# Kernel tuning notes

Hardware: AMD Instinct MI355X
Metric: run time of the kernel (lower is better)

Reference implementation:

```python
import jax, jax.numpy as jnp
import numpy as np

DIM = 1024
NQ = 16
NKV = 4
HD = DIM // NQ  # 64
HID = 2048
E = 8
B, S = 1, 1024
EPS = 1e-6


def rmsnorm(x, w):
    ms = jnp.mean(x * x, axis=-1, keepdims=True)
    return w * (x * jax.lax.rsqrt(ms + EPS))


def rope_tables(seq_len, head_dim):
    inv_freq = 1.0 / (10000.0 ** (jnp.arange(0, head_dim, 2, dtype=jnp.float32) / head_dim))
    t = jnp.arange(seq_len, dtype=jnp.float32)
    freqs = jnp.einsum('i,j->ij', t, inv_freq)  # [S, HD/2]
    return jnp.cos(freqs), jnp.sin(freqs)


def apply_rope(x, cos, sin):
    # x: [B, S, H, HD]; cos/sin: [S, HD/2]
    c = cos[None, :, None, :]
    s = sin[None, :, None, :]
    half = x.shape[-1] // 2
    x1, x2 = x[..., :half], x[..., half:]
    return jnp.concatenate([x1 * c - x2 * s, x1 * s + x2 * c], axis=-1)


def setup_inputs() -> dict:
    key = jax.random.key(0)
    ks = jax.random.split(key, 20)
    sc = lambda fan_in: 1.0 / np.sqrt(fan_in)
    d = {}
    d['x'] = jax.random.normal(ks[0], (B, S, DIM), dtype=jnp.float32)
    d['ln1_w'] = jnp.ones((DIM,), jnp.float32)
    d['ln2_w'] = jnp.ones((DIM,), jnp.float32)
    d['Wq'] = jax.random.normal(ks[1], (DIM, DIM), jnp.float32) * sc(DIM)
    d['bq'] = jnp.zeros((DIM,), jnp.float32)
    d['Wk'] = jax.random.normal(ks[2], (DIM, HD * NKV), jnp.float32) * sc(DIM)
    d['bk'] = jnp.zeros((HD * NKV,), jnp.float32)
    d['Wv'] = jax.random.normal(ks[3], (DIM, HD * NKV), jnp.float32) * sc(DIM)
    d['bv'] = jnp.zeros((HD * NKV,), jnp.float32)
    d['qn_w'] = jnp.ones((HD,), jnp.float32)
    d['kn_w'] = jnp.ones((HD,), jnp.float32)
    d['Wg'] = jax.random.normal(ks[4], (HD, HD), jnp.float32) * sc(HD)
    d['bg'] = jnp.zeros((HD,), jnp.float32)
    d['Wo'] = jax.random.normal(ks[5], (DIM, DIM), jnp.float32) * sc(DIM)
    d['bo'] = jnp.zeros((DIM,), jnp.float32)
    d['Wr'] = jax.random.normal(ks[6], (DIM, E), jnp.float32) * sc(DIM)
    d['br'] = jnp.zeros((E,), jnp.float32)
    d['W1'] = jax.random.normal(ks[7], (E, DIM, 2 * HID), jnp.float32) * sc(DIM)
    d['b1'] = jnp.zeros((E, 2 * HID), jnp.float32)
    d['W2'] = jax.random.normal(ks[8], (E, HID, DIM), jnp.float32) * sc(HID)
    d['b2'] = jnp.zeros((E, DIM), jnp.float32)
    return d


def _forward(x, ln1_w, ln2_w, Wq, bq, Wk, bk, Wv, bv, qn_w, kn_w, Wg, bg, Wo, bo,
             Wr, br, W1, b1, W2, b2):
    batch, seq, _ = x.shape
    cos, sin = rope_tables(seq, HD)

    # --- attention ---
    h = rmsnorm(x, ln1_w)
    q = (h @ Wq + bq).reshape(batch, seq, NQ, HD)
    k = (h @ Wk + bk).reshape(batch, seq, NKV, HD)
    v = (h @ Wv + bv).reshape(batch, seq, NKV, HD)
    q = rmsnorm(apply_rope(q, cos, sin), qn_w)
    k = rmsnorm(apply_rope(k, cos, sin), kn_w)
    rep = NQ // NKV
    k = jnp.repeat(k, rep, axis=2)  # [B,S,NQ,HD]
    v = jnp.repeat(v, rep, axis=2)
    scores = jnp.einsum('bthd,bshd->bhts', q, k) / np.sqrt(HD)
    causal = jnp.tril(jnp.ones((seq, seq), dtype=bool))
    scores = jnp.where(causal[None, None], scores, -jnp.inf)
    attn = jax.nn.softmax(scores, axis=-1)
    out = jnp.einsum('bhts,bshd->bthd', attn, v)
    gate = jax.nn.sigmoid(out @ Wg + bg)
    out = (out * gate).reshape(batch, seq, DIM)
    x = x + out @ Wo + bo

    # --- top-1 MoE (note: output is NOT scaled by router probs) ---
    h2 = rmsnorm(x, ln2_w)
    logits = h2 @ Wr + br  # [B,S,E]
    top1 = jnp.argmax(logits, axis=-1).reshape(-1)  # [T]
    xt = h2.reshape(-1, DIM)  # [T,DIM]
    # dense dispatch: run all experts, gather the chosen one
    u = jnp.einsum('td,edf->tef', xt, W1) + b1  # [T,E,2H]
    u1, u2 = u[..., :HID], u[..., HID:]
    act = u1 * jax.nn.sigmoid(u2)  # SwiGLU
    y_all = jnp.einsum('teh,ehd->ted', act, W2) + b2  # [T,E,DIM]
    y = jnp.take_along_axis(y_all, top1[:, None, None], axis=1)[:, 0, :]
    return x + y.reshape(batch, seq, DIM)


def reference(x, ln1_w, ln2_w, Wq, bq, Wk, bk, Wv, bv, qn_w, kn_w, Wg, bg, Wo, bo,
              Wr, br, W1, b1, W2, b2):
    return _forward(x, ln1_w, ln2_w, Wq, bq, Wk, bk, Wv, bv, qn_w, kn_w,
                    Wg, bg, Wo, bo, Wr, br, W1, b1, W2, b2)
```

## Files before the change

kernel.cpp:

```cpp
#include <hip/hip_runtime.h>
#include <hip/hip_bf16.h>
#include <cstddef>

#define DIM 1024
#define NQ 16
#define NKV 4
#define HD 64
#define HID 2048
#define NE 8
#define SEQ 1024
#define EPSF 1e-6f
#define MAX_TILES 24
#define GST 72

typedef __hip_bfloat16 bf16;
typedef __attribute__((ext_vector_type(8))) short short8;
typedef __attribute__((ext_vector_type(4))) float floatx4;

typedef union { short8 s; unsigned int u[4]; } s8u;

__device__ __forceinline__ unsigned int f2b(float f) {
    union { bf16 b; unsigned short s; } u;
    u.b = __float2bfloat16(f);
    return (unsigned int)u.s;
}
__device__ __forceinline__ unsigned int pk2(float a, float b) {
    return f2b(a) | (f2b(b) << 16);
}

__device__ __forceinline__ void touch_f32(const float* __restrict__ p,
                                          size_t nlines, size_t gid, size_t step)
{
    float acc = 0.f;
    for (size_t i = gid; i < nlines; i += step)
        acc += p[i << 5];
    asm volatile("" :: "v"(acc));
}

__global__ __launch_bounds__(256) void rmsnorm_kernel(const float* __restrict__ src,
                                                      const float* __restrict__ w,
                                                      float* __restrict__ dst)
{
    int row = blockIdx.x, tid = threadIdx.x;
    __shared__ float red[256];
    float vals[4];
    float sq = 0.f;
    size_t base = (size_t)row * DIM;
    #pragma unroll
    for (int i = 0; i < 4; i++) {
        int idx = tid + i * 256;
        float v = src[base + idx];
        vals[i] = v; sq += v * v;
    }
    red[tid] = sq; __syncthreads();
    for (int s = 128; s > 0; s >>= 1) {
        if (tid < s) red[tid] += red[tid + s];
        __syncthreads();
    }
    float rs = 1.0f / sqrtf(red[0] * (1.0f / DIM) + EPSF);
    #pragma unroll
    for (int i = 0; i < 4; i++) {
        int idx = tid + i * 256;
        dst[base + idx] = w[idx] * vals[i] * rs;
    }
}

template<int NB>
__global__ __launch_bounds__(256) void gemm_t(
    const float* __restrict__ A, const float* __restrict__ B, const float* __restrict__ bias,
    float* __restrict__ C, const float* __restrict__ resf,
    const int* __restrict__ perm, const int* __restrict__ tile_expert,
    int N, int K, int mode)
{
    constexpr int KR = NB / 4;
    constexpr int NT = NB / 16;
    __shared__ short As[64 * GST];
    __shared__ short Bs[NB * GST];
    int tid = threadIdx.x;
    int mbase = blockIdx.y * 64, nbase = blockIdx.x * NB;

    size_t Beoff = 0, biasoff = 0;
    if (tile_expert) {
        int e = tile_expert[blockIdx.y];
        if (e < 0) return;
        Beoff = (size_t)e * K * N;
        biasoff = (size_t)e * N;
    }

    int ar = tid >> 4, ak = (tid & 15) << 2;
    int bn = tid & (NB - 1), bkk = (tid / NB) * KR;
    const float* BpBase = B + Beoff + (size_t)bkk * N + nbase + bn;

    int wv = tid >> 6, ln = tid & 63;
    int fm = (wv << 4) + (ln & 15);
    int fn = ln & 15;
    int fk = (ln >> 4) << 3;

    floatx4 acc[NT];
    #pragma unroll
    for (int nt = 0; nt < NT; nt++)
        #pragma unroll
        for (int r = 0; r < 4; r++) acc[nt][r] = 0.f;

    float4 apre[4];
    float bpre[KR];
    #pragma unroll
    for (int p = 0; p < 4; p++)
        apre[p] = *(const float4*)(A + (size_t)(mbase + (p << 4) + ar) * K + ak);
    #pragma unroll
    for (int i = 0; i < KR; i++)
        bpre[i] = BpBase[(size_t)i * N];

    for (int kt = 0; kt < K; kt += 64) {
        #pragma unroll
        for (int p = 0; p < 4; p++) {
            int m = (p << 4) + ar;
            uint2 wpk; wpk.x = pk2(apre[p].x, apre[p].y); wpk.y = pk2(apre[p].z, apre[p].w);
            *(uint2*)&As[m * GST + ak] = wpk;
        }
        #pragma unroll
        for (int i2 = 0; i2 < KR; i2 += 8) {
            unsigned int u[4];
            #pragma unroll
            for (int i = 0; i < 4; i++)
                u[i] = pk2(bpre[i2 + 2 * i], bpre[i2 + 2 * i + 1]);
            *(uint4*)&Bs[bn * GST + bkk + i2] = make_uint4(u[0], u[1], u[2], u[3]);
        }
        __syncthreads();

        int kn = kt + 64;
        if (kn < K) {
            #pragma unroll
            for (int p = 0; p < 4; p++)
                apre[p] = *(const float4*)(A + (size_t)(mbase + (p << 4) + ar) * K + kn + ak);
            const float* bp = BpBase + (size_t)kn * N;
            #pragma unroll
            for (int i = 0; i < KR; i++) bpre[i] = bp[(size_t)i * N];
        }

        #pragma unroll
        for (int ks = 0; ks < 2; ks++) {
            short8 af = *(const short8*)&As[fm * GST + (ks << 5) + fk];
            #pragma unroll
            for (int nt = 0; nt < NT; nt++) {
                short8 bf = *(const short8*)&Bs[((nt << 4) + fn) * GST + (ks << 5) + fk];
                acc[nt] = __builtin_amdgcn_mfma_f32_16x16x32_bf16(af, bf, acc[nt], 0, 0, 0);
            }
        }
        __syncthreads();
    }

    int rowb = mbase + (wv << 4) + ((ln >> 4) << 2);
    if (mode == 2) {
        int tk[4];
        #pragma unroll
        for (int r = 0; r < 4; r++) tk[r] = perm[rowb + r];
        #pragma unroll
        for (int nt = 0; nt < NT; nt++) {
            int col = nbase + (nt << 4) + fn;
            float bsv = bias[biasoff + col];
            #pragma unroll
            for (int r = 0; r < 4; r++)
                if (tk[r] >= 0)
                    C[(size_t)tk[r] * N + col] = resf[(size_t)tk[r] * N + col] + acc[nt][r] + bsv;
        }
    } else {
        #pragma unroll
        for (int nt = 0; nt < NT; nt++) {
            int col = nbase + (nt << 4) + fn;
            float bsv = bias[col];
            #pragma unroll
            for (int r = 0; r < 4; r++) {
                float vv = acc[nt][r] + bsv;
                if (mode == 1) vv += resf[(size_t)(rowb + r) * N + col];
                C[(size_t)(rowb + r) * N + col] = vv;
            }
        }
    }
}

__global__ __launch_bounds__(256) void qkv_kernel(
    const float* __restrict__ A,
    const float* __restrict__ Wq, const float* __restrict__ bq,
    const float* __restrict__ Wk, const float* __restrict__ bk,
    const float* __restrict__ Wv, const float* __restrict__ bv,
    const float* __restrict__ Wwarm,
    float* __restrict__ qo, float* __restrict__ ko, float* __restrict__ vo)
{
    constexpr int NB = 32, KR = 8, NT = 2;
    int tid = threadIdx.x;
    int bx = blockIdx.x;

    if (bx >= 48) {
        size_t gid  = ((size_t)(bx - 48) * gridDim.y + blockIdx.y) * 256 + tid;
        size_t step = (size_t)64 * gridDim.y * 256;
        touch_f32(Wwarm, (size_t)NE * DIM * (2 * HID) / 32, gid, step);
        return;
    }

    __shared__ short As[64 * GST];
    __shared__ short Bs[NB * GST];
    int mbase = blockIdx.y * 64;

    const float* B; const float* bias; float* C; int N, nbase;
    if (bx < 32)      { B = Wq; bias = bq; C = qo; N = DIM;      nbase = bx * 32; }
    else if (bx < 40) { B = Wk; bias = bk; C = ko; N = NKV * HD; nbase = (bx - 32) * 32; }
    else              { B = Wv; bias = bv; C = vo; N = NKV * HD; nbase = (bx - 40) * 32; }

    int ar = tid >> 4, ak = (tid & 15) << 2;
    int bn = tid & (NB - 1), bkk = (tid / NB) * KR;
    const float* BpBase = B + (size_t)bkk * N + nbase + bn;

    int wv = tid >> 6, ln = tid & 63;
    int fm = (wv << 4) + (ln & 15);
    int fn = ln & 15;
    int fk = (ln >> 4) << 3;

    floatx4 acc[NT];
    #pragma unroll
    for (int nt = 0; nt < NT; nt++)
        #pragma unroll
        for (int r = 0; r < 4; r++) acc[nt][r] = 0.f;

    float4 apre[4];
    float bpre[KR];
    #pragma unroll
    for (int p = 0; p < 4; p++)
        apre[p] = *(const float4*)(A + (size_t)(mbase + (p << 4) + ar) * DIM + ak);
    #pragma unroll
    for (int i = 0; i < KR; i++)
        bpre[i] = BpBase[(size_t)i * N];

    for (int kt = 0; kt < DIM; kt += 64) {
        #pragma unroll
        for (int p = 0; p < 4; p++) {
            int m = (p << 4) + ar;
            uint2 wpk; wpk.x = pk2(apre[p].x, apre[p].y); wpk.y = pk2(apre[p].z, apre[p].w);
            *(uint2*)&As[m * GST + ak] = wpk;
        }
        {
            unsigned int u[4];
            #pragma unroll
            for (int i = 0; i < 4; i++)
                u[i] = pk2(bpre[2 * i], bpre[2 * i + 1]);
            *(uint4*)&Bs[bn * GST + bkk] = make_uint4(u[0], u[1], u[2], u[3]);
        }
        __syncthreads();

        int kn = kt + 64;
        if (kn < DIM) {
            #pragma unroll
            for (int p = 0; p < 4; p++)
                apre[p] = *(const float4*)(A + (size_t)(mbase + (p << 4) + ar) * DIM + kn + ak);
            const float* bp = BpBase + (size_t)kn * N;
            #pragma unroll
            for (int i = 0; i < KR; i++) bpre[i] = bp[(size_t)i * N];
        }

        #pragma unroll
        for (int ks = 0; ks < 2; ks++) {
            short8 af = *(const short8*)&As[fm * GST + (ks << 5) + fk];
            #pragma unroll
            for (int nt = 0; nt < NT; nt++) {
                short8 bf = *(const short8*)&Bs[((nt << 4) + fn) * GST + (ks << 5) + fk];
                acc[nt] = __builtin_amdgcn_mfma_f32_16x16x32_bf16(af, bf, acc[nt], 0, 0, 0);
            }
        }
        __syncthreads();
    }

    int rowb = mbase + (wv << 4) + ((ln >> 4) << 2);
    #pragma unroll
    for (int nt = 0; nt < NT; nt++) {
        int col = nbase + (nt << 4) + fn;
        float bsv = bias[col];
        #pragma unroll
        for (int r = 0; r < 4; r++)
            C[(size_t)(rowb + r) * N + col] = acc[nt][r] + bsv;
    }
}

__global__ __launch_bounds__(256) void moe1_kernel(
    const float* __restrict__ A,
    const float* __restrict__ W1,
    const float* __restrict__ b1,
    float* __restrict__ act,
    const int* __restrict__ perm,
    const int* __restrict__ tile_expert)
{
    constexpr int NB = 32, KR = 8, NT = 2;
    __shared__ short As[64 * GST];
    __shared__ short B1s[NB * GST];
    __shared__ short B2s[NB * GST];
    int tid = threadIdx.x;
    int mbase = blockIdx.y * 64, nbase = blockIdx.x * NB;
    int e = tile_expert[blockIdx.y];
    if (e < 0) return;
    const float* Wp = W1 + (size_t)e * DIM * (2 * HID);
    const float* bp1 = b1 + (size_t)e * (2 * HID);

    int ar = tid >> 4, ak = (tid & 15) << 2;
    int tok[4];
    #pragma unroll
    for (int p = 0; p < 4; p++) tok[p] = perm[mbase + (p << 4) + ar];

    int bn = tid & (NB - 1), bkk = (tid / NB) * KR;
    const float* BpBase = Wp + (size_t)bkk * (2 * HID) + nbase + bn;

    int wv = tid >> 6, ln = tid & 63;
    int fm = (wv << 4) + (ln & 15);
    int fn = ln & 15;
    int fk = (ln >> 4) << 3;

    floatx4 acc1[NT], acc2[NT];
    #pragma unroll
    for (int nt = 0; nt < NT; nt++)
        #pragma unroll
        for (int r = 0; r < 4; r++) { acc1[nt][r] = 0.f; acc2[nt][r] = 0.f; }

    float4 apre[4];
    float b1pre[KR], b2pre[KR];
    #pragma unroll
    for (int p = 0; p < 4; p++)
        apre[p] = (tok[p] >= 0)
            ? *(const float4*)(A + (size_t)tok[p] * DIM + ak)
            : make_float4(0.f, 0.f, 0.f, 0.f);
    #pragma unroll
    for (int i = 0; i < KR; i++) {
        b1pre[i] = BpBase[(size_t)i * (2 * HID)];
        b2pre[i] = BpBase[(size_t)i * (2 * HID) + HID];
    }

    for (int kt = 0; kt < DIM; kt += 64) {
        #pragma unroll
        for (int p = 0; p < 4; p++) {
            int m = (p << 4) + ar;
            uint2 wpk; wpk.x = pk2(apre[p].x, apre[p].y); wpk.y = pk2(apre[p].z, apre[p].w);
            *(uint2*)&As[m * GST + ak] = wpk;
        }
        {
            unsigned int u1[4], u2[4];
            #pragma unroll
            for (int i = 0; i < 4; i++) {
                u1[i] = pk2(b1pre[2 * i], b1pre[2 * i + 1]);
                u2[i] = pk2(b2pre[2 * i], b2pre[2 * i + 1]);
            }
            *(uint4*)&B1s[bn * GST + bkk] = make_uint4(u1[0], u1[1], u1[2], u1[3]);
            *(uint4*)&B2s[bn * GST + bkk] = make_uint4(u2[0], u2[1], u2[2], u2[3]);
        }
        __syncthreads();

        int kn = kt + 64;
        if (kn < DIM) {
            #pragma unroll
            for (int p = 0; p < 4; p++)
                apre[p] = (tok[p] >= 0)
                    ? *(const float4*)(A + (size_t)tok[p] * DIM + kn + ak)
                    : make_float4(0.f, 0.f, 0.f, 0.f);
            const float* bp = BpBase + (size_t)kn * (2 * HID);
            #pragma unroll
            for (int i = 0; i < KR; i++) {
                b1pre[i] = bp[(size_t)i * (2 * HID)];
                b2pre[i] = bp[(size_t)i * (2 * HID) + HID];
            }
        }

        #pragma unroll
        for (int ks = 0; ks < 2; ks++) {
            short8 af = *(const short8*)&As[fm * GST + (ks << 5) + fk];
            #pragma unroll
            for (int nt = 0; nt < NT; nt++) {
                int bo = ((nt << 4) + fn) * GST + (ks << 5) + fk;
                short8 bf1 = *(const short8*)&B1s[bo];
                short8 bf2 = *(const short8*)&B2s[bo];
                acc1[nt] = __builtin_amdgcn_mfma_f32_16x16x32_bf16(af, bf1, acc1[nt], 0, 0, 0);
                acc2[nt] = __builtin_amdgcn_mfma_f32_16x16x32_bf16(af, bf2, acc2[nt], 0, 0, 0);
            }
        }
        __syncthreads();
    }

    int rowb = mbase + (wv << 4) + ((ln >> 4) << 2);
    #pragma unroll
    for (int nt = 0; nt < NT; nt++) {
        int col = nbase + (nt << 4) + fn;
        float bs1 = bp1[col];
        float bs2 = bp1[HID + col];
        #pragma unroll
        for (int r = 0; r < 4; r++) {
            float u1 = acc1[nt][r] + bs1;
            float u2 = acc2[nt][r] + bs2;
            act[(size_t)(rowb + r) * HID + col] = u1 * (1.0f / (1.0f + expf(-u2)));
        }
    }
}

__global__ __launch_bounds__(64) void rope_rms_kernel(float* __restrict__ qb,
                                                      float* __restrict__ kb,
                                                      const float* __restrict__ qnw,
                                                      const float* __restrict__ knw)
{
    int t = blockIdx.x, hy = blockIdx.y, d = threadIdx.x;
    float* x; const float* w; int nh, h;
    if (hy < NQ) { x = qb; w = qnw; nh = NQ;  h = hy; }
    else         { x = kb; w = knw; nh = NKV; h = hy - NQ; }
    int base = (t * nh + h) * HD;
    int i = d & 31;
    float x1 = x[base + i];
    float x2 = x[base + 32 + i];
    float inv = 1.0f / powf(10000.0f, (float)(2 * i) * (1.0f / HD));
    float fr = (float)t * inv;
    float c = cosf(fr), s = sinf(fr);
    float r = (d < 32) ? (x1 * c - x2 * s) : (x1 * s + x2 * c);
    float sq = r * r;
    #pragma unroll
    for (int m = 32; m >= 1; m >>= 1) sq += __shfl_xor(sq, m);
    float rs = 1.0f / sqrtf(sq * (1.0f / HD) + EPSF);
    __syncthreads();
    x[base + d] = r * rs * w[d];
}

__global__ __launch_bounds__(256) void fattn_kernel(const float* __restrict__ q,
                                                    const float* __restrict__ k,
                                                    const float* __restrict__ v,
                                                    const float* __restrict__ Wg,
                                                    const float* __restrict__ bg,
                                                    const float* __restrict__ W2warm,
                                                    float* __restrict__ o)
{
    int h = blockIdx.x;
    int tid = threadIdx.x;

    if (h >= NQ) {
        size_t gid  = ((size_t)(h - NQ) * gridDim.y + blockIdx.y) * 256 + tid;
        size_t step = (size_t)32 * gridDim.y * 256;
        touch_f32(W2warm, (size_t)NE * HID * DIM / 32, gid, step);
        return;
    }

    __shared__ short lds[2][2][64 * GST];

    int qt = blockIdx.y;
    int kvh = h >> 2;
    int w = tid >> 6, ln = tid & 63;
    int c = ln & 15, g = ln >> 4;
    int qbase = qt * 64;
    const size_t krow = (size_t)NKV * HD;

    short8 qf[2];
    {
        const float* qp = q + ((size_t)(qbase + 16 * w + c) * NQ + h) * HD + 8 * g;
        #pragma unroll
        for (int ks = 0; ks < 2; ks++) {
            float4 a = *(const float4*)(qp + 32 * ks);
            float4 b = *(const float4*)(qp + 32 * ks + 4);
            s8u t;
            t.u[0] = pk2(a.x * 0.125f, a.y * 0.125f);
            t.u[1] = pk2(a.z * 0.125f, a.w * 0.125f);
            t.u[2] = pk2(b.x * 0.125f, b.y * 0.125f);
            t.u[3] = pk2(b.z * 0.125f, b.w * 0.125f);
            qf[ks] = t.s;
        }
    }

    int kr[4], kd4[4];
    #pragma unroll
    for (int i = 0; i < 4; i++) { int f4 = tid + 256 * i; kr[i] = f4 >> 4; kd4[i] = f4 & 15; }
    int vd = tid & 63, vrb = (tid >> 6) << 4;

    float4 kreg[4];
    float vreg[16];
    {
        const float* kb = k + (size_t)kvh * HD;
        #pragma unroll
        for (int i = 0; i < 4; i++)
            kreg[i] = *(const float4*)(kb + (size_t)kr[i] * krow + kd4[i] * 4);
        const float* vb = v + (size_t)kvh * HD + vd;
        #pragma unroll
        for (int i = 0; i < 16; i++)
            vreg[i] = vb[(size_t)(vrb + i) * krow];
    }

    float m_i = -INFINITY, l_i = 0.f;
    floatx4 ot[4];
    #pragma unroll
    for (int mt = 0; mt < 4; mt++)
        #pragma unroll
        for (int r = 0; r < 4; r++) ot[mt][r] = 0.f;

    for (int kt = 0; kt <= qt; kt++) {
        short* KB = lds[kt & 1][0];
        short* VT = lds[kt & 1][1];

        #pragma unroll
        for (int i = 0; i < 4; i++) {
            uint2 wp; wp.x = pk2(kreg[i].x, kreg[i].y); wp.y = pk2(kreg[i].z, kreg[i].w);
            *(uint2*)&KB[kr[i] * GST + kd4[i] * 4] = wp;
        }
        {
            unsigned int u[8];
            #pragma unroll
            for (int i = 0; i < 8; i++) u[i] = pk2(vreg[2 * i], vreg[2 * i + 1]);
            *(uint4*)&VT[vd * GST + vrb]     = make_uint4(u[0], u[1], u[2], u[3]);
            *(uint4*)&VT[vd * GST + vrb + 8] = make_uint4(u[4], u[5], u[6], u[7]);
        }
        __syncthreads();

        if (kt < qt) {
            int kb2 = (kt + 1) * 64;
            const float* kb = k + ((size_t)kb2 * NKV + kvh) * HD;
            #pragma unroll
            for (int i = 0; i < 4; i++)
                kreg[i] = *(const float4*)(kb + (size_t)kr[i] * krow + kd4[i] * 4);
            const float* vp = v + ((size_t)kb2 * NKV + kvh) * HD + vd;
            #pragma unroll
            for (int i = 0; i < 16; i++)
                vreg[i] = vp[(size_t)(vrb + i) * krow];
        }

        float p[4][4];
        #pragma unroll
        for (int mt = 0; mt < 4; mt++) {
            floatx4 s = {0.f, 0.f, 0.f, 0.f};
            #pragma unroll
            for (int ks = 0; ks < 2; ks++) {
                short8 kf = *(const short8*)&KB[(16 * mt + c) * GST + 32 * ks + 8 * g];
                s = __builtin_amdgcn_mfma_f32_16x16x32_bf16(kf, qf[ks], s, 0, 0, 0);
            }
            #pragma unroll
            for (int r = 0; r < 4; r++) p[mt][r] = s[r];
        }

        if (kt == qt) {
            #pragma unroll
            for (int mt = 0; mt < 4; mt++)
                #pragma unroll
                for (int r = 0; r < 4; r++)
                    if (16 * mt + 4 * g + r > 16 * w + c) p[mt][r] = -1e30f;
        }

        float tm = p[0][0];
        #pragma unroll
        for (int mt = 0; mt < 4; mt++)
            #pragma unroll
            for (int r = 0; r < 4; r++) tm = fmaxf(tm, p[mt][r]);
        tm = fmaxf(tm, __shfl_xor(tm, 16));
        tm = fmaxf(tm, __shfl_xor(tm, 32));
        float mn = fmaxf(m_i, tm);
        float alpha = __expf(m_i - mn);
        float ts = 0.f;
        #pragma unroll
        for (int mt = 0; mt < 4; mt++)
            #pragma unroll
            for (int r = 0; r < 4; r++) {
                float e = __expf(p[mt][r] - mn);
                p[mt][r] = e; ts += e;
            }
        ts += __shfl_xor(ts, 16);
        ts += __shfl_xor(ts, 32);
        l_i = alpha * l_i + ts;
        m_i = mn;
        #pragma unroll
        for (int mt = 0; mt < 4; mt++)
            #pragma unroll
            for (int r = 0; r < 4; r++) ot[mt][r] *= alpha;

        unsigned int pd[4][2];
        #pragma unroll
        for (int mt = 0; mt < 4; mt++) {
            pd[mt][0] = pk2(p[mt][0], p[mt][1]);
            pd[mt][1] = pk2(p[mt][2], p[mt][3]);
        }

        int srcA = c + ((ln & 16) << 1);
        int srcB = srcA + 16;
        int gh = g >> 1;
        short8 pf[2];
        #pragma unroll
        for (int ks = 0; ks < 2; ks++) {
            s8u t;
            unsigned int a0 = (unsigned)__shfl((int)pd[2 * ks][0],     srcA);
            unsigned int a1 = (unsigned)__shfl((int)pd[2 * ks + 1][0], srcA);
            t.u[0] = gh ? a1 : a0;
            unsigned int b0 = (unsigned)__shfl((int)pd[2 * ks][1],     srcA);
            unsigned int b1 = (unsigned)__shfl((int)pd[2 * ks + 1][1], srcA);
            t.u[1] = gh ? b1 : b0;
            unsigned int c0 = (unsigned)__shfl((int)pd[2 * ks][0],     srcB);
            unsigned int c1 = (unsigned)__shfl((int)pd[2 * ks + 1][0], srcB);
            t.u[2] = gh ? c1 : c0;
            unsigned int d0 = (unsigned)__shfl((int)pd[2 * ks][1],     srcB);
            unsigned int d1 = (unsigned)__shfl((int)pd[2 * ks + 1][1], srcB);
            t.u[3] = gh ? d1 : d0;
            pf[ks] = t.s;
        }

        #pragma unroll
        for (int mt = 0; mt < 4; mt++) {
            #pragma unroll
            for (int ks = 0; ks < 2; ks++) {
                short8 vf = *(const short8*)&VT[(16 * mt + c) * GST + 32 * ks + 8 * g];
                ot[mt] = __builtin_amdgcn_mfma_f32_16x16x32_bf16(vf, pf[ks], ot[mt], 0, 0, 0);
            }
        }
    }

    __syncthreads();
    float* L   = (float*)lds;
    float* WgS = L + 64 * 68;

    int we = tid >> 2, wd = (tid & 3) << 4;
    float4 wg4[4];
    #pragma unroll
    for (int i = 0; i < 4; i++)
        wg4[i] = *(const float4*)(Wg + (size_t)we * HD + wd + 4 * i);

    float rl = 1.0f / l_i;
    #pragma unroll
    for (int mt = 0; mt < 4; mt++)
        #pragma unroll
        for (int r = 0; r < 4; r++)
            L[(16 * w + c) * 68 + 16 * mt + 4 * g + r] = ot[mt][r] * rl;
    #pragma unroll
    for (int i = 0; i < 4; i++)
        *(float4*)&WgS[we * 68 + wd + 4 * i] = wg4[i];
    __syncthreads();

    int r = tid >> 2, d0 = (tid & 3) << 4;
    float4 a0 = *(const float4*)(bg + d0);
    float4 a1 = *(const float4*)(bg + d0 + 4);
    float4 a2 = *(const float4*)(bg + d0 + 8);
    float4 a3 = *(const float4*)(bg + d0 + 12);
    for (int e = 0; e < HD; e++) {
        float ov = L[r * 68 + e];
        float4 w0 = *(const float4*)&WgS[e * 68 + d0];
        float4 w1 = *(const float4*)&WgS[e * 68 + d0 + 4];
        float4 w2 = *(const float4*)&WgS[e * 68 + d0 + 8];
        float4 w3 = *(const float4*)&WgS[e * 68 + d0 + 12];
        a0.x += ov * w0.x; a0.y += ov * w0.y; a0.z += ov * w0.z; a0.w += ov * w0.w;
        a1.x += ov * w1.x; a1.y += ov * w1.y; a1.z += ov * w1.z; a1.w += ov * w1.w;
        a2.x += ov * w2.x; a2.y += ov * w2.y; a2.z += ov * w2.z; a2.w += ov * w2.w;
        a3.x += ov * w3.x; a3.y += ov * w3.y; a3.z += ov * w3.z; a3.w += ov * w3.w;
    }
    float* op = o + ((size_t)(qbase + r) * NQ + h) * HD + d0;
    float4 av[4] = {a0, a1, a2, a3};
    #pragma unroll
    for (int i = 0; i < 4; i++) {
        float4 ov4 = *(const float4*)&L[r * 68 + d0 + 4 * i];
        float4 res;
        res.x = ov4.x / (1.0f + expf(-av[i].x));
        res.y = ov4.y / (1.0f + expf(-av[i].y));
        res.z = ov4.z / (1.0f + expf(-av[i].z));
        res.w = ov4.w / (1.0f + expf(-av[i].w));
        *(float4*)(op + 4 * i) = res;
    }
}

__global__ __launch_bounds__(64) void router_kernel(const float* __restrict__ h2,
                                                    const float* __restrict__ Wr,
                                                    const float* __restrict__ br,
                                                    int* __restrict__ top1)
{
    int t = blockIdx.x, lane = threadIdx.x;
    float acc[NE] = {0.f, 0.f, 0.f, 0.f, 0.f, 0.f, 0.f, 0.f};
    for (int d = lane; d < DIM; d += 64) {
        float hv = h2[(size_t)t * DIM + d];
        float4 w0 = *(const float4*)(Wr + (size_t)d * NE);
        float4 w1 = *(const float4*)(Wr + (size_t)d * NE + 4);
        acc[0] += hv * w0.x; acc[1] += hv * w0.y;
        acc[2] += hv * w0.z; acc[3] += hv * w0.w;
        acc[4] += hv * w1.x; acc[5] += hv * w1.y;
        acc[6] += hv * w1.z; acc[7] += hv * w1.w;
    }
    #pragma unroll
    for (int e = 0; e < NE; e++)
        for (int off = 32; off >= 1; off >>= 1) acc[e] += __shfl_down(acc[e], off);
    if (lane == 0) {
        float best = acc[0] + br[0]; int be = 0;
        #pragma unroll
        for (int e = 1; e < NE; e++) {
            float l = acc[e] + br[e];
            if (l > best) { best = l; be = e; }
        }
        top1[t] = be;
    }
}

__global__ __launch_bounds__(64) void bucket_kernel(const int* __restrict__ top1,
                                                    int* __restrict__ perm,
                                                    int* __restrict__ tile_expert)
{
    int lane = threadIdx.x;

    int e_of[16];
    {
        const int4* tp = (const int4*)(top1 + lane * 16);
        #pragma unroll
        for (int c = 0; c < 4; c++) {
            int4 v = tp[c];
            e_of[c * 4 + 0] = v.x & 7;
            e_of[c * 4 + 1] = v.y & 7;
            e_of[c * 4 + 2] = v.z & 7;
            e_of[c * 4 + 3] = v.w & 7;
        }
    }

    int cnt[NE];
    #pragma unroll
    for (int e = 0; e < NE; e++) {
        int c = 0;
        #pragma unroll
        for (int i = 0; i < 16; i++) c += (e_of[i] == e) ? 1 : 0;
        cnt[e] = c;
    }

    int pre[NE];
    #pragma unroll
    for (int e = 0; e < NE; e++) pre[e] = cnt[e];
    #pragma unroll
    for (int off = 1; off < 64; off <<= 1) {
        #pragma unroll
        for (int e = 0; e < NE; e++) {
            int t = __shfl_up(pre[e], off);
            if (lane >= off) pre[e] += t;
        }
    }
    int tot[NE];
    #pragma unroll
    for (int e = 0; e < NE; e++) {
        tot[e] = __shfl(pre[e], 63);
        pre[e] -= cnt[e];
    }

    int off_e[NE + 1];
    off_e[0] = 0;
    #pragma unroll
    for (int e = 0; e < NE; e++)
        off_e[e + 1] = off_e[e] + (((tot[e] + 63) >> 6) << 6);

    if (lane < MAX_TILES) {
        int tb = lane << 6;
        int te = -1;
        #pragma unroll
        for (int e = 0; e < NE; e++)
            if (tb >= off_e[e] && tb < off_e[e + 1]) te = e;
        tile_expert[lane] = te;
    }

    #pragma unroll
    for (int e = 0; e < NE; e++)
        for (int i = off_e[e] + tot[e] + lane; i < off_e[e + 1]; i += 64)
            perm[i] = -1;

    #pragma unroll
    for (int e = 0; e < NE; e++) {
        int pos = off_e[e] + pre[e];
        #pragma unroll
        for (int i = 0; i < 16; i++) {
            if (e_of[i] == e) { perm[pos] = lane * 16 + i; pos++; }
        }
    }
}

extern "C" void kernel_launch(void* const* d_in, const int* in_sizes, int n_in,
                              void* d_out, int out_size, void* d_ws, size_t ws_size,
                              hipStream_t stream)
{
    const float* x    = (const float*)d_in[0];
    const float* ln1w = (const float*)d_in[1];
    const float* ln2w = (const float*)d_in[2];
    const float* Wq   = (const float*)d_in[3];
    const float* bq   = (const float*)d_in[4];
    const float* Wk   = (const float*)d_in[5];
    const float* bk   = (const float*)d_in[6];
    const float* Wv   = (const float*)d_in[7];
    const float* bv   = (const float*)d_in[8];
    const float* qnw  = (const float*)d_in[9];
    const float* knw  = (const float*)d_in[10];
    const float* Wg   = (const float*)d_in[11];
    const float* bg   = (const float*)d_in[12];
    const float* Wo   = (const float*)d_in[13];
    const float* bo   = (const float*)d_in[14];
    const float* Wr   = (const float*)d_in[15];
    const float* br   = (const float*)d_in[16];
    const float* W1   = (const float*)d_in[17];
    const float* b1   = (const float*)d_in[18];
    const float* W2   = (const float*)d_in[19];
    const float* b2   = (const float*)d_in[20];
    float* out = (float*)d_out;
    (void)in_sizes; (void)n_in; (void)out_size; (void)ws_size;

    char* ws = (char*)d_ws;
    float* h    = (float*)(ws);
    float* q    = (float*)(ws + ((size_t)4  << 20));
    float* kbuf = (float*)(ws + ((size_t)8  << 20));
    float* vbuf = (float*)(ws + ((size_t)9  << 20));
    float* ao   = (float*)(ws + ((size_t)10 << 20));
    float* x2   = (float*)(ws);
    float* h2   = (float*)(ws + ((size_t)4  << 20));
    float* act  = (float*)(ws + ((size_t)24 << 20));
    int* top1   = (int*)  (ws + ((size_t)44 << 20));
    int* perm   = top1 + 2048;
    int* texp   = perm + MAX_TILES * 64;

    rmsnorm_kernel<<<SEQ, 256, 0, stream>>>(x, ln1w, h);
    qkv_kernel<<<dim3(48 + 64, SEQ / 64), 256, 0, stream>>>(
        h, Wq, bq, Wk, bk, Wv, bv, W1, q, kbuf, vbuf);
    rope_rms_kernel<<<dim3(SEQ, NQ + NKV), 64, 0, stream>>>(q, kbuf, qnw, knw);
    fattn_kernel<<<dim3(NQ + 32, SEQ / 64), 256, 0, stream>>>(
        q, kbuf, vbuf, Wg, bg, W2, ao);
    gemm_t<32><<<dim3(DIM / 32, SEQ / 64), 256, 0, stream>>>(
        ao, Wo, bo, x2, x, nullptr, nullptr, DIM, DIM, 1);
    rmsnorm_kernel<<<SEQ, 256, 0, stream>>>(x2, ln2w, h2);
    router_kernel<<<SEQ, 64, 0, stream>>>(h2, Wr, br, top1);
    bucket_kernel<<<1, 64, 0, stream>>>(top1, perm, texp);
    moe1_kernel<<<dim3(HID / 32, MAX_TILES), 256, 0, stream>>>(
        h2, W1, b1, act, perm, texp);
    gemm_t<32><<<dim3(DIM / 32, MAX_TILES), 256, 0, stream>>>(
        act, W2, b2, out, x2, perm, texp, DIM, HID, 2);
}
```

Before: 451.5 us.

## Convert MoE expert weights to bf16 in side blocks and read bf16 in MoE GEMMs

Earlier kernels already spent spare blocks touching the MoE weights to warm the cache. Those blocks now convert W1 and W2 from fp32 to bf16 into workspace buffers. The MoE GEMMs then load 16-bit weights instead of fp32, halving weight traffic, and a dedicated bf16-B kernel replaces the generic gemm_t for the second expert GEMM. The cost is that the side blocks now read 256 MB of fp32 weights in full and write 128 MB of bf16 every call, where before they touched only one float per line. That extra work may stretch the qkv and attention kernels.

```diff
diff --git a/kernel.cpp b/kernel.cpp
--- a/kernel.cpp
+++ b/kernel.cpp
@@ -28,13 +28,19 @@
     return f2b(a) | (f2b(b) << 16);
 }
 
-__device__ __forceinline__ void touch_f32(const float* __restrict__ p,
-                                          size_t nlines, size_t gid, size_t step)
-{
-    float acc = 0.f;
-    for (size_t i = gid; i < nlines; i += step)
-        acc += p[i << 5];
-    asm volatile("" :: "v"(acc));
+__device__ __forceinline__ void conv_b16(const float* __restrict__ src,
+                                         unsigned short* __restrict__ dst,
+                                         size_t n8, size_t gid, size_t step)
+{
+    for (size_t i = gid; i < n8; i += step) {
+        const float* s = src + (i << 3);
+        float4 a = *(const float4*)(s);
+        float4 b = *(const float4*)(s + 4);
+        uint4 o;
+        o.x = pk2(a.x, a.y); o.y = pk2(a.z, a.w);
+        o.z = pk2(b.x, b.y); o.w = pk2(b.z, b.w);
+        *(uint4*)(dst + (i << 3)) = o;
+    }
 }
 
 __global__ __launch_bounds__(256) void rmsnorm_kernel(const float* __restrict__ src,
@@ -179,12 +185,108 @@
     }
 }
 
+__global__ __launch_bounds__(256) void gemm2b_kernel(
+    const float* __restrict__ A,
+    const unsigned short* __restrict__ B,
+    const float* __restrict__ bias,
+    float* __restrict__ C, const float* __restrict__ resf,
+    const int* __restrict__ perm, const int* __restrict__ tile_expert)
+{
+    constexpr int NB = 32, KR = 8, NT = 2;
+    const int N = DIM, K = HID;
+    __shared__ short As[64 * GST];
+    __shared__ short Bs[NB * GST];
+    int tid = threadIdx.x;
+    int mbase = blockIdx.y * 64, nbase = blockIdx.x * NB;
+
+    int e = tile_expert[blockIdx.y];
+    if (e < 0) return;
+    const unsigned short* Bp = B + (size_t)e * K * N;
+    const float* bp_bias = bias + (size_t)e * N;
+
+    int ar = tid >> 4, ak = (tid & 15) << 2;
+    int bn = tid & (NB - 1), bkk = (tid / NB) * KR;
+    const unsigned short* BpBase = Bp + (size_t)bkk * N + nbase + bn;
+
+    int wv = tid >> 6, ln = tid & 63;
+    int fm = (wv << 4) + (ln & 15);
+    int fn = ln & 15;
+    int fk = (ln >> 4) << 3;
+
+    floatx4 acc[NT];
+    #pragma unroll
+    for (int nt = 0; nt < NT; nt++)
+        #pragma unroll
+        for (int r = 0; r < 4; r++) acc[nt][r] = 0.f;
+
+    float4 apre[4];
+    unsigned short bpre[KR];
+    #pragma unroll
+    for (int p = 0; p < 4; p++)
+        apre[p] = *(const float4*)(A + (size_t)(mbase + (p << 4) + ar) * K + ak);
+    #pragma unroll
+    for (int i = 0; i < KR; i++)
+        bpre[i] = BpBase[(size_t)i * N];
+
+    for (int kt = 0; kt < K; kt += 64) {
+        #pragma unroll
+        for (int p = 0; p < 4; p++) {
+            int m = (p << 4) + ar;
+            uint2 wpk; wpk.x = pk2(apre[p].x, apre[p].y); wpk.y = pk2(apre[p].z, apre[p].w);
+            *(uint2*)&As[m * GST + ak] = wpk;
+        }
+        {
+            unsigned int u[4];
+            #pragma unroll
+            for (int i = 0; i < 4; i++)
+                u[i] = (unsigned int)bpre[2 * i] | ((unsigned int)bpre[2 * i + 1] << 16);
+            *(uint4*)&Bs[bn * GST + bkk] = make_uint4(u[0], u[1], u[2], u[3]);
+        }
+        __syncthreads();
+
+        int kn = kt + 64;
+        if (kn < K) {
+            #pragma unroll
+            for (int p = 0; p < 4; p++)
+                apre[p] = *(const float4*)(A + (size_t)(mbase + (p << 4) + ar) * K + kn + ak);
+            const unsigned short* bp = BpBase + (size_t)kn * N;
+            #pragma unroll
+            for (int i = 0; i < KR; i++) bpre[i] = bp[(size_t)i * N];
+        }
+
+        #pragma unroll
+        for (int ks = 0; ks < 2; ks++) {
+            short8 af = *(const short8*)&As[fm * GST + (ks << 5) + fk];
+            #pragma unroll
+            for (int nt = 0; nt < NT; nt++) {
+                short8 bf = *(const short8*)&Bs[((nt << 4) + fn) * GST + (ks << 5) + fk];
+                acc[nt] = __builtin_amdgcn_mfma_f32_16x16x32_bf16(af, bf, acc[nt], 0, 0, 0);
+            }
+        }
+        __syncthreads();
+    }
+
+    int rowb = mbase + (wv << 4) + ((ln >> 4) << 2);
+    int tk[4];
+    #pragma unroll
+    for (int r = 0; r < 4; r++) tk[r] = perm[rowb + r];
+    #pragma unroll
+    for (int nt = 0; nt < NT; nt++) {
+        int col = nbase + (nt << 4) + fn;
+        float bsv = bp_bias[col];
+        #pragma unroll
+        for (int r = 0; r < 4; r++)
+            if (tk[r] >= 0)
+                C[(size_t)tk[r] * N + col] = resf[(size_t)tk[r] * N + col] + acc[nt][r] + bsv;
+    }
+}
+
 __global__ __launch_bounds__(256) void qkv_kernel(
     const float* __restrict__ A,
     const float* __restrict__ Wq, const float* __restrict__ bq,
     const float* __restrict__ Wk, const float* __restrict__ bk,
     const float* __restrict__ Wv, const float* __restrict__ bv,
-    const float* __restrict__ Wwarm,
+    const float* __restrict__ W1f, unsigned short* __restrict__ w1b,
     float* __restrict__ qo, float* __restrict__ ko, float* __restrict__ vo)
 {
     constexpr int NB = 32, KR = 8, NT = 2;
@@ -194,7 +296,7 @@
     if (bx >= 48) {
         size_t gid  = ((size_t)(bx - 48) * gridDim.y + blockIdx.y) * 256 + tid;
         size_t step = (size_t)64 * gridDim.y * 256;
-        touch_f32(Wwarm, (size_t)NE * DIM * (2 * HID) / 32, gid, step);
+        conv_b16(W1f, w1b, (size_t)NE * DIM * (2 * HID) / 8, gid, step);
         return;
     }
 
@@ -282,7 +384,7 @@
 
 __global__ __launch_bounds__(256) void moe1_kernel(
     const float* __restrict__ A,
-    const float* __restrict__ W1,
+    const unsigned short* __restrict__ W1,
     const float* __restrict__ b1,
     float* __restrict__ act,
     const int* __restrict__ perm,
@@ -296,7 +398,7 @@
     int mbase = blockIdx.y * 64, nbase = blockIdx.x * NB;
     int e = tile_expert[blockIdx.y];
     if (e < 0) return;
-    const float* Wp = W1 + (size_t)e * DIM * (2 * HID);
+    const unsigned short* Wp = W1 + (size_t)e * DIM * (2 * HID);
     const float* bp1 = b1 + (size_t)e * (2 * HID);
 
     int ar = tid >> 4, ak = (tid & 15) << 2;
@@ -305,7 +407,7 @@
     for (int p = 0; p < 4; p++) tok[p] = perm[mbase + (p << 4) + ar];
 
     int bn = tid & (NB - 1), bkk = (tid / NB) * KR;
-    const float* BpBase = Wp + (size_t)bkk * (2 * HID) + nbase + bn;
+    const unsigned short* BpBase = Wp + (size_t)bkk * (2 * HID) + nbase + bn;
 
     int wv = tid >> 6, ln = tid & 63;
     int fm = (wv << 4) + (ln & 15);
@@ -319,7 +421,7 @@
         for (int r = 0; r < 4; r++) { acc1[nt][r] = 0.f; acc2[nt][r] = 0.f; }
 
     float4 apre[4];
-    float b1pre[KR], b2pre[KR];
+    unsigned short b1pre[KR], b2pre[KR];
     #pragma unroll
     for (int p = 0; p < 4; p++)
         apre[p] = (tok[p] >= 0)
@@ -342,8 +444,8 @@
             unsigned int u1[4], u2[4];
             #pragma unroll
             for (int i = 0; i < 4; i++) {
-                u1[i] = pk2(b1pre[2 * i], b1pre[2 * i + 1]);
-                u2[i] = pk2(b2pre[2 * i], b2pre[2 * i + 1]);
+                u1[i] = (unsigned int)b1pre[2 * i] | ((unsigned int)b1pre[2 * i + 1] << 16);
+                u2[i] = (unsigned int)b2pre[2 * i] | ((unsigned int)b2pre[2 * i + 1] << 16);
             }
             *(uint4*)&B1s[bn * GST + bkk] = make_uint4(u1[0], u1[1], u1[2], u1[3]);
             *(uint4*)&B2s[bn * GST + bkk] = make_uint4(u2[0], u2[1], u2[2], u2[3]);
@@ -357,7 +459,7 @@
                 apre[p] = (tok[p] >= 0)
                     ? *(const float4*)(A + (size_t)tok[p] * DIM + kn + ak)
                     : make_float4(0.f, 0.f, 0.f, 0.f);
-            const float* bp = BpBase + (size_t)kn * (2 * HID);
+            const unsigned short* bp = BpBase + (size_t)kn * (2 * HID);
             #pragma unroll
             for (int i = 0; i < KR; i++) {
                 b1pre[i] = bp[(size_t)i * (2 * HID)];
@@ -425,7 +527,8 @@
                                                     const float* __restrict__ v,
                                                     const float* __restrict__ Wg,
                                                     const float* __restrict__ bg,
-                                                    const float* __restrict__ W2warm,
+                                                    const float* __restrict__ W2f,
+                                                    unsigned short* __restrict__ w2b,
                                                     float* __restrict__ o)
 {
     int h = blockIdx.x;
@@ -434,7 +537,7 @@
     if (h >= NQ) {
         size_t gid  = ((size_t)(h - NQ) * gridDim.y + blockIdx.y) * 256 + tid;
         size_t step = (size_t)32 * gridDim.y * 256;
-        touch_f32(W2warm, (size_t)NE * HID * DIM / 32, gid, step);
+        conv_b16(W2f, w2b, (size_t)NE * HID * DIM / 8, gid, step);
         return;
     }
 
@@ -801,20 +904,22 @@
     int* top1   = (int*)  (ws + ((size_t)44 << 20));
     int* perm   = top1 + 2048;
     int* texp   = perm + MAX_TILES * 64;
+    unsigned short* w1b = (unsigned short*)(ws + ((size_t)64  << 20));
+    unsigned short* w2b = (unsigned short*)(ws + ((size_t)128 << 20));
 
     rmsnorm_kernel<<<SEQ, 256, 0, stream>>>(x, ln1w, h);
     qkv_kernel<<<dim3(48 + 64, SEQ / 64), 256, 0, stream>>>(
-        h, Wq, bq, Wk, bk, Wv, bv, W1, q, kbuf, vbuf);
+        h, Wq, bq, Wk, bk, Wv, bv, W1, w1b, q, kbuf, vbuf);
     rope_rms_kernel<<<dim3(SEQ, NQ + NKV), 64, 0, stream>>>(q, kbuf, qnw, knw);
     fattn_kernel<<<dim3(NQ + 32, SEQ / 64), 256, 0, stream>>>(
-        q, kbuf, vbuf, Wg, bg, W2, ao);
+        q, kbuf, vbuf, Wg, bg, W2, w2b, ao);
     gemm_t<32><<<dim3(DIM / 32, SEQ / 64), 256, 0, stream>>>(
         ao, Wo, bo, x2, x, nullptr, nullptr, DIM, DIM, 1);
     rmsnorm_kernel<<<SEQ, 256, 0, stream>>>(x2, ln2w, h2);
     router_kernel<<<SEQ, 64, 0, stream>>>(h2, Wr, br, top1);
     bucket_kernel<<<1, 64, 0, stream>>>(top1, perm, texp);
     moe1_kernel<<<dim3(HID / 32, MAX_TILES), 256, 0, stream>>>(
-        h2, W1, b1, act, perm, texp);
-    gemm_t<32><<<dim3(DIM / 32, MAX_TILES), 256, 0, stream>>>(
-        act, W2, b2, out, x2, perm, texp, DIM, HID, 2);
-}
+        h2, w1b, b1, act, perm, texp);
+    gemm2b_kernel<<<dim3(DIM / 32, MAX_TILES), 256, 0, stream>>>(
+        act, w2b, b2, out, x2, perm, texp);
+}
```

New measurement: 467.2 us. +3.5%, slower.
